# Performance work log

Measured on AMD Instinct MI355X. Metric: run time of the kernel, lower is better.

## Reference

```python
import jax, jax.numpy as jnp
import numpy as np

B, T, DIN, H = 8, 4096, 1024, 2048
INIT_SCALE = 0.1


def setup_inputs() -> dict:
    key = jax.random.key(0)
    ks = jax.random.split(key, 5)
    x = jax.random.normal(ks[0], (B, T, DIN), dtype=jnp.float32)
    Wi = jax.random.normal(ks[1], (H, DIN), dtype=jnp.float32) * INIT_SCALE
    Wg = jax.random.normal(ks[2], (H, DIN), dtype=jnp.float32) * INIT_SCALE
    Wo = jax.random.normal(ks[3], (DIN, H), dtype=jnp.float32) * INIT_SCALE
    log_a = jax.random.normal(ks[4], (H,), dtype=jnp.float32) * INIT_SCALE - 1.0
    bi = jnp.zeros((H,), dtype=jnp.float32)
    bg = jnp.zeros((H,), dtype=jnp.float32)
    bo = jnp.zeros((DIN,), dtype=jnp.float32)
    return {"x": x, "Wi": Wi, "bi": bi, "Wg": Wg, "bg": bg,
            "Wo": Wo, "bo": bo, "log_a": log_a}


def _lru_forward(x, Wi, bi, Wg, bg, Wo, bo, log_a):
    # u, gate: (B, T, H)
    u = jnp.einsum('btd,hd->bth', x, Wi) + bi
    gate = jax.nn.sigmoid(jnp.einsum('btd,hd->bth', x, Wg) + bg)
    a = jax.nn.sigmoid(log_a)  # (H,) diagonal recurrence coefficient

    # diagonal linear recurrence h_t = a*h_{t-1} + u_t, scanned over time
    def step(h, u_t):
        h = a * h + u_t
        return h, h

    u_tbh = jnp.swapaxes(u, 0, 1)  # (T, B, H)
    h0 = jnp.zeros((x.shape[0], log_a.shape[0]), dtype=x.dtype)
    _, h_seq = jax.lax.scan(step, h0, u_tbh)  # (T, B, H)
    h_seq = jnp.swapaxes(h_seq, 0, 1)  # (B, T, H)

    y = jnp.einsum('bth,dh->btd', h_seq * gate, Wo) + bo
    return y


def reference(x, Wi, bi, Wg, bg, Wo, bo, log_a):
    return _lru_forward(x, Wi, bi, Wg, bg, Wo, bo, log_a)
```

## Files before the change

### kernel.cpp

```cpp
#include <hip/hip_runtime.h>
#include <hip/hip_bf16.h>
#include <stdint.h>

using bf16 = __hip_bfloat16;

typedef short bf16x8 __attribute__((ext_vector_type(8)));
typedef float f32x4 __attribute__((ext_vector_type(4)));

__device__ __forceinline__ float bf2f(bf16 x) { return __bfloat162float(x); }
__device__ __forceinline__ bf16 f2bf(float x) { return __float2bfloat16(x); }

__device__ __forceinline__ void async_load16(const bf16* gptr, bf16* lptr) {
    __builtin_amdgcn_global_load_lds(
        (const __attribute__((address_space(1))) void*)gptr,
        (__attribute__((address_space(3))) void*)lptr,
        16, 0, 0);
}

__device__ __forceinline__ void wg_barrier() {
    asm volatile("" ::: "memory");
    __builtin_amdgcn_s_barrier();
    asm volatile("" ::: "memory");
}

#define VMCNT(n) asm volatile("s_waitcnt vmcnt(" #n ")" ::: "memory")

template <int MODE>
__global__ __launch_bounds__(512, 2) void gemm256(
    const bf16* __restrict__ A, const bf16* __restrict__ Bt,
    const float* __restrict__ bias, void* __restrict__ Cout,
    int M, int N, int K)
{
    __shared__ bf16 lds[2 * 2 * 32 * 512];

    const int tid  = threadIdx.x;
    const int wid  = tid >> 6;
    const int lane = tid & 63;
    const int wm = wid >> 2;
    const int wn = wid & 3;

    const int nwg = gridDim.x;
    const int q8 = nwg >> 3, r8 = nwg & 7;
    const int xcd = blockIdx.x & 7, loc = blockIdx.x >> 3;
    const int wgid = (xcd < r8 ? xcd * (q8 + 1) : r8 * (q8 + 1) + (xcd - r8) * q8) + loc;
    const int ntn = N >> 8;
    const int bx = wgid % ntn;
    const int by = wgid / ntn;
    const int m0 = by * 256;
    const int n0 = bx * 256;

    const bf16* Ablk = A  + (size_t)m0 * K;
    const bf16* Bblk = Bt + (size_t)n0 * K;

    const int frow = lane & 15;
    const int fq   = lane >> 4;
    const int roff = frow * 32 + ((fq ^ ((frow >> 1) & 3)) * 8);

    const int swl  = lane ^ ((lane >> 3) & 3);
    const int srow = swl >> 2;
    const int scol = (swl & 3) * 8;

    const int rgA = (wid & 3) + ((wid & 4) << 1);
    const int rgB = (wid & 1) + ((wid & 2) << 1) + ((wid & 4) << 1);

    auto stageA = [&](int buf, int k0, int q) {
        const int rg = rgA + q * 4;
        const bf16* g = Ablk + (size_t)(rg * 16 + srow) * K + (k0 + scol);
        bf16* l = &lds[buf * 32768 + rg * 1024];
        async_load16(g, l);
        async_load16(g + 32, l + 512);
    };
    auto stageB = [&](int buf, int k0, int q) {
        const int rg = rgB + q * 2;
        const bf16* g = Bblk + (size_t)(rg * 16 + srow) * K + (k0 + scol);
        bf16* l = &lds[buf * 32768 + 16384 + rg * 1024];
        async_load16(g, l);
        async_load16(g + 32, l + 512);
    };

    f32x4 acc[8][4];
#pragma unroll
    for (int i = 0; i < 8; ++i)
#pragma unroll
        for (int j = 0; j < 4; ++j)
            acc[i][j] = f32x4{0.f, 0.f, 0.f, 0.f};

    bf16x8 af[4][2];
    bf16x8 bfr[2][2][2];

    auto LDA = [&](int buf, int ih) {
#pragma unroll
        for (int i = 0; i < 4; ++i)
#pragma unroll
            for (int kk = 0; kk < 2; ++kk)
                af[i][kk] = *(const bf16x8*)&lds[buf * 32768 +
                    ((wm * 8 + ih * 4 + i) * 2 + kk) * 512 + roff];
    };
    auto LDB = [&](int buf, int jh) {
#pragma unroll
        for (int j = 0; j < 2; ++j)
#pragma unroll
            for (int kk = 0; kk < 2; ++kk)
                bfr[jh][j][kk] = *(const bf16x8*)&lds[buf * 32768 + 16384 +
                    ((wn * 4 + jh * 2 + j) * 2 + kk) * 512 + roff];
    };
    auto MFMAQ = [&](int ih, int jh) {
        __builtin_amdgcn_s_setprio(1);
#pragma unroll
        for (int kk = 0; kk < 2; ++kk)
#pragma unroll
            for (int i = 0; i < 4; ++i)
#pragma unroll
                for (int j = 0; j < 2; ++j)
                    acc[ih * 4 + i][jh * 2 + j] =
                        __builtin_amdgcn_mfma_f32_16x16x32_bf16(
                            af[i][kk], bfr[jh][j][kk],
                            acc[ih * 4 + i][jh * 2 + j], 0, 0, 0);
        __builtin_amdgcn_s_setprio(0);
    };

    stageA(0, 0, 0);
    stageB(0, 0, 1);
    stageA(0, 0, 1);
    stageB(0, 0, 0);
    stageA(1, 64, 0);
    stageB(1, 64, 1);
    VMCNT(4);
    wg_barrier();

    const int NT = K >> 6;
    for (int t = 0; t < NT; t += 2) {
        const int k1 = (t + 1) << 6;
        const int k2 = (t + 2 < NT ? t + 2 : NT - 1) << 6;
        const int k3 = (t + 3 < NT ? t + 3 : NT - 1) << 6;

        LDA(0, 0); LDB(0, 0);
        stageA(1, k1, 1);
        wg_barrier();
        MFMAQ(0, 0);
        LDB(0, 1);
        stageB(1, k1, 0);
        wg_barrier();
        MFMAQ(0, 1);
        LDA(0, 1);
        stageA(0, k2, 0);
        wg_barrier();
        MFMAQ(1, 1);
        stageB(0, k2, 1);
        VMCNT(4);
        wg_barrier();
        MFMAQ(1, 0);
        LDA(1, 0); LDB(1, 0);
        stageA(0, k2, 1);
        wg_barrier();
        MFMAQ(0, 0);
        LDB(1, 1);
        stageB(0, k2, 0);
        wg_barrier();
        MFMAQ(0, 1);
        LDA(1, 1);
        stageA(1, k3, 0);
        wg_barrier();
        MFMAQ(1, 1);
        stageB(1, k3, 1);
        VMCNT(4);
        wg_barrier();
        MFMAQ(1, 0);
    }
    asm volatile("s_waitcnt vmcnt(0)" ::: "memory");

    const int crow = fq * 4;
    const int ccol = frow;
    float bv[4];
#pragma unroll
    for (int j = 0; j < 4; ++j) bv[j] = bias[n0 + wn * 64 + 16 * j + ccol];
#pragma unroll
    for (int i = 0; i < 8; ++i) {
#pragma unroll
        for (int r = 0; r < 4; ++r) {
            const int row = m0 + wm * 128 + 16 * i + crow + r;
#pragma unroll
            for (int j = 0; j < 4; ++j) {
                const int col = n0 + wn * 64 + 16 * j + ccol;
                float v = acc[i][j][r] + bv[j];
                if constexpr (MODE == 1) v = 1.f / (1.f + __expf(-v));
                if constexpr (MODE == 2)
                    ((float*)Cout)[(size_t)row * N + col] = v;
                else
                    ((bf16*)Cout)[(size_t)row * N + col] = f2bf(v);
            }
        }
    }
}

#define SCAN_T 4096
#define SCAN_H 2048
#define SCAN_B 8
#define SCAN_L 512
#define SCAN_W 64

__global__ __launch_bounds__(256) void lru_scan(
    const bf16* __restrict__ u, bf16* gs, const float* __restrict__ asig)
{
    const int tid   = blockIdx.x * 256 + threadIdx.x;
    const int h     = tid & (SCAN_H - 1);
    const int rem   = tid >> 11;
    const int b     = rem & (SCAN_B - 1);
    const int chunk = rem >> 3;

    const float a = asig[h];
    const size_t base = (size_t)b * SCAN_T * SCAN_H + h;
    const bf16* up = u + base;
    bf16* gp = gs + base;

    const int t1 = chunk * SCAN_L;
    const int warm0 = (chunk == 0) ? 0 : SCAN_W;

    float hs = 0.f;
    for (int t = t1 - warm0; t < t1; t += 8) {
        float uv[8];
#pragma unroll
        for (int i = 0; i < 8; ++i) uv[i] = bf2f(up[(size_t)(t + i) * SCAN_H]);
#pragma unroll
        for (int i = 0; i < 8; ++i) hs = fmaf(a, hs, uv[i]);
    }
    for (int t = t1; t < t1 + SCAN_L; t += 8) {
        float uv[8], gv[8];
#pragma unroll
        for (int i = 0; i < 8; ++i) {
            uv[i] = bf2f(up[(size_t)(t + i) * SCAN_H]);
            gv[i] = bf2f(gp[(size_t)(t + i) * SCAN_H]);
        }
#pragma unroll
        for (int i = 0; i < 8; ++i) {
            hs = fmaf(a, hs, uv[i]);
            gp[(size_t)(t + i) * SCAN_H] = f2bf(hs * gv[i]);
        }
    }
}

__global__ void cvt_f32_bf16_x4(const float* __restrict__ in,
                                bf16* __restrict__ out, int n4)
{
    const int i = blockIdx.x * blockDim.x + threadIdx.x;
    if (i >= n4) return;
    const float4 v = ((const float4*)in)[i];
    bf16 h[4] __attribute__((aligned(8)));
    h[0] = f2bf(v.x); h[1] = f2bf(v.y); h[2] = f2bf(v.z); h[3] = f2bf(v.w);
    ((uint64_t*)out)[i] = *(const uint64_t*)h;
}

__global__ void sigmoid_vec(const float* __restrict__ in,
                            float* __restrict__ out, int n)
{
    const int i = blockIdx.x * blockDim.x + threadIdx.x;
    if (i < n) out[i] = 1.f / (1.f + __expf(-in[i]));
}

extern "C" void kernel_launch(void* const* d_in, const int* in_sizes, int n_in,
                              void* d_out, int out_size, void* d_ws, size_t ws_size,
                              hipStream_t stream)
{
    const float* x     = (const float*)d_in[0];
    const float* Wi    = (const float*)d_in[1];
    const float* bi    = (const float*)d_in[2];
    const float* Wg    = (const float*)d_in[3];
    const float* bg    = (const float*)d_in[4];
    const float* Wo    = (const float*)d_in[5];
    const float* bo    = (const float*)d_in[6];
    const float* log_a = (const float*)d_in[7];
    float* y = (float*)d_out;

    constexpr int Bc = 8, T = 4096, DIN = 1024, H = 2048;
    constexpr int M = Bc * T;

    char* ws = (char*)d_ws;
    size_t off = 0;
    auto alloc = [&](size_t bytes) -> void* {
        void* p = ws + off;
        off += (bytes + 255) & ~(size_t)255;
        return p;
    };
    bf16*  xb   = (bf16*)alloc((size_t)M * DIN * 2);
    bf16*  wib  = (bf16*)alloc((size_t)H * DIN * 2);
    bf16*  wgb  = (bf16*)alloc((size_t)H * DIN * 2);
    bf16*  wob  = (bf16*)alloc((size_t)DIN * H * 2);
    float* asig = (float*)alloc((size_t)H * 4);
    bf16*  u    = (bf16*)alloc((size_t)M * H * 2);
    bf16*  g    = (bf16*)alloc((size_t)M * H * 2);
    (void)ws_size; (void)in_sizes; (void)n_in; (void)out_size;

    {
        const int n4 = M * DIN / 4;
        cvt_f32_bf16_x4<<<(n4 + 255) / 256, 256, 0, stream>>>(x, xb, n4);
        const int w4 = H * DIN / 4;
        cvt_f32_bf16_x4<<<(w4 + 255) / 256, 256, 0, stream>>>(Wi, wib, w4);
        cvt_f32_bf16_x4<<<(w4 + 255) / 256, 256, 0, stream>>>(Wg, wgb, w4);
        cvt_f32_bf16_x4<<<(w4 + 255) / 256, 256, 0, stream>>>(Wo, wob, w4);
        sigmoid_vec<<<(H + 255) / 256, 256, 0, stream>>>(log_a, asig, H);
    }

    gemm256<0><<<(M / 256) * (H / 256), 512, 0, stream>>>(xb, wib, bi, u, M, H, DIN);
    gemm256<1><<<(M / 256) * (H / 256), 512, 0, stream>>>(xb, wgb, bg, g, M, H, DIN);

    lru_scan<<<(Bc * H * (T / SCAN_L)) / 256, 256, 0, stream>>>(u, g, asig);

    gemm256<2><<<(M / 256) * (DIN / 256), 512, 0, stream>>>(g, wob, bo, y, M, DIN, H);
}
```

Baseline: 726.4 us.

## Shrink GEMM tile to 256x128 with 4 waves and single-buffer LDS pipeline

Changes the GEMM workgroup from 512 threads with a 256x256 tile and double-buffered LDS (128KB) to 256 threads with a 256x128 tile and a single 64KB LDS buffer. The A tile's second half alternates between two slots so the next k-tile can be staged while the current one is consumed. The intent is to cut LDS use so more workgroups fit per CU and to double the grid size for better load balance. In exchange, each output element gets less reuse of the loaded data and the schedule has more barriers per k-step and less prefetch depth.

```diff
diff --git a/kernel.cpp b/kernel.cpp
--- a/kernel.cpp
+++ b/kernel.cpp
@@ -26,28 +26,28 @@
 #define VMCNT(n) asm volatile("s_waitcnt vmcnt(" #n ")" ::: "memory")
 
 template <int MODE>
-__global__ __launch_bounds__(512, 2) void gemm256(
+__global__ __launch_bounds__(256, 2) void gemm256(
     const bf16* __restrict__ A, const bf16* __restrict__ Bt,
     const float* __restrict__ bias, void* __restrict__ Cout,
     int M, int N, int K)
 {
-    __shared__ bf16 lds[2 * 2 * 32 * 512];
+    __shared__ bf16 lds[32768];
 
     const int tid  = threadIdx.x;
     const int wid  = tid >> 6;
     const int lane = tid & 63;
-    const int wm = wid >> 2;
-    const int wn = wid & 3;
+    const int wm = wid >> 1;
+    const int wn = wid & 1;
 
     const int nwg = gridDim.x;
     const int q8 = nwg >> 3, r8 = nwg & 7;
     const int xcd = blockIdx.x & 7, loc = blockIdx.x >> 3;
     const int wgid = (xcd < r8 ? xcd * (q8 + 1) : r8 * (q8 + 1) + (xcd - r8) * q8) + loc;
-    const int ntn = N >> 8;
+    const int ntn = N >> 7;
     const int bx = wgid % ntn;
     const int by = wgid / ntn;
     const int m0 = by * 256;
-    const int n0 = bx * 256;
+    const int n0 = bx * 128;
 
     const bf16* Ablk = A  + (size_t)m0 * K;
     const bf16* Bblk = Bt + (size_t)n0 * K;
@@ -60,23 +60,24 @@
     const int srow = swl >> 2;
     const int scol = (swl & 3) * 8;
 
-    const int rgA = (wid & 3) + ((wid & 4) << 1);
-    const int rgB = (wid & 1) + ((wid & 2) << 1) + ((wid & 4) << 1);
-
-    auto stageA = [&](int buf, int k0, int q) {
-        const int rg = rgA + q * 4;
-        const bf16* g = Ablk + (size_t)(rg * 16 + srow) * K + (k0 + scol);
-        bf16* l = &lds[buf * 32768 + rg * 1024];
+    auto stageA = [&](int k0, int q, int slot) {
+#pragma unroll
+        for (int rr = 0; rr < 2; ++rr) {
+            const int r = wid * 2 + rr;
+            const int p = (r & 3) + q * 4 + ((r >> 2) << 3);
+            const bf16* g = Ablk + (size_t)(p * 16 + srow) * K + (k0 + scol);
+            bf16* l = (q == 1 && slot) ? &lds[24576 + r * 1024] : &lds[p * 1024];
+            async_load16(g, l);
+            async_load16(g + 32, l + 512);
+        }
+    };
+    auto stageB = [&](int k0, int q) {
+        const int p = (wid & 1) + ((wid >> 1) << 2) + q * 2;
+        const bf16* g = Bblk + (size_t)(p * 16 + srow) * K + (k0 + scol);
+        bf16* l = &lds[16384 + p * 1024];
         async_load16(g, l);
         async_load16(g + 32, l + 512);
     };
-    auto stageB = [&](int buf, int k0, int q) {
-        const int rg = rgB + q * 2;
-        const bf16* g = Bblk + (size_t)(rg * 16 + srow) * K + (k0 + scol);
-        bf16* l = &lds[buf * 32768 + 16384 + rg * 1024];
-        async_load16(g, l);
-        async_load16(g + 32, l + 512);
-    };
 
     f32x4 acc[8][4];
 #pragma unroll
@@ -88,21 +89,30 @@
     bf16x8 af[4][2];
     bf16x8 bfr[2][2][2];
 
-    auto LDA = [&](int buf, int ih) {
+    auto LDA0 = [&]() {
 #pragma unroll
         for (int i = 0; i < 4; ++i)
 #pragma unroll
             for (int kk = 0; kk < 2; ++kk)
-                af[i][kk] = *(const bf16x8*)&lds[buf * 32768 +
-                    ((wm * 8 + ih * 4 + i) * 2 + kk) * 512 + roff];
-    };
-    auto LDB = [&](int buf, int jh) {
+                af[i][kk] = *(const bf16x8*)&lds[(wm * 8 + i) * 1024 + kk * 512 + roff];
+    };
+    auto LDA1 = [&](int slot) {
+#pragma unroll
+        for (int i = 0; i < 4; ++i) {
+            const int base = slot ? (24576 + (wm * 4 + i) * 1024)
+                                  : ((wm * 8 + 4 + i) * 1024);
+#pragma unroll
+            for (int kk = 0; kk < 2; ++kk)
+                af[i][kk] = *(const bf16x8*)&lds[base + kk * 512 + roff];
+        }
+    };
+    auto LDB = [&](int jh) {
 #pragma unroll
         for (int j = 0; j < 2; ++j)
 #pragma unroll
             for (int kk = 0; kk < 2; ++kk)
-                bfr[jh][j][kk] = *(const bf16x8*)&lds[buf * 32768 + 16384 +
-                    ((wn * 4 + jh * 2 + j) * 2 + kk) * 512 + roff];
+                bfr[jh][j][kk] = *(const bf16x8*)&lds[16384 +
+                    (wn * 4 + jh * 2 + j) * 1024 + kk * 512 + roff];
     };
     auto MFMAQ = [&](int ih, int jh) {
         __builtin_amdgcn_s_setprio(1);
@@ -119,55 +129,39 @@
         __builtin_amdgcn_s_setprio(0);
     };
 
+    const int NT = K >> 6;
+
+    stageA(0, 1, 0);
     stageA(0, 0, 0);
-    stageB(0, 0, 1);
-    stageA(0, 0, 1);
-    stageB(0, 0, 0);
-    stageA(1, 64, 0);
-    stageB(1, 64, 1);
-    VMCNT(4);
+    stageB(0, 0);
+    stageB(0, 1);
+    VMCNT(2);
     wg_barrier();
-
-    const int NT = K >> 6;
-    for (int t = 0; t < NT; t += 2) {
-        const int k1 = (t + 1) << 6;
-        const int k2 = (t + 2 < NT ? t + 2 : NT - 1) << 6;
-        const int k3 = (t + 3 < NT ? t + 3 : NT - 1) << 6;
-
-        LDA(0, 0); LDB(0, 0);
-        stageA(1, k1, 1);
+    LDA0(); LDB(0);
+    VMCNT(0);
+    wg_barrier();
+
+    for (int t = 0; t < NT; ++t) {
+        const int kn = (t + 1 < NT ? t + 1 : NT - 1) << 6;
+        const int sl = (t + 1) & 1;
+        MFMAQ(0, 0);
+        LDB(1);
         wg_barrier();
-        MFMAQ(0, 0);
-        LDB(0, 1);
-        stageB(1, k1, 0);
+        stageA(kn, 1, sl);
+        stageA(kn, 0, 0);
+        stageB(kn, 0);
+        MFMAQ(0, 1);
+        LDA1(t & 1);
         wg_barrier();
-        MFMAQ(0, 1);
-        LDA(0, 1);
-        stageA(0, k2, 0);
-        wg_barrier();
+        stageB(kn, 1);
         MFMAQ(1, 1);
-        stageB(0, k2, 1);
-        VMCNT(4);
+        VMCNT(2);
         wg_barrier();
         MFMAQ(1, 0);
-        LDA(1, 0); LDB(1, 0);
-        stageA(0, k2, 1);
+        LDA0(); LDB(0);
+        VMCNT(0);
         wg_barrier();
-        MFMAQ(0, 0);
-        LDB(1, 1);
-        stageB(0, k2, 0);
-        wg_barrier();
-        MFMAQ(0, 1);
-        LDA(1, 1);
-        stageA(1, k3, 0);
-        wg_barrier();
-        MFMAQ(1, 1);
-        stageB(1, k3, 1);
-        VMCNT(4);
-        wg_barrier();
-        MFMAQ(1, 0);
-    }
-    asm volatile("s_waitcnt vmcnt(0)" ::: "memory");
+    }
 
     const int crow = fq * 4;
     const int ccol = frow;
@@ -300,10 +294,10 @@
         sigmoid_vec<<<(H + 255) / 256, 256, 0, stream>>>(log_a, asig, H);
     }
 
-    gemm256<0><<<(M / 256) * (H / 256), 512, 0, stream>>>(xb, wib, bi, u, M, H, DIN);
-    gemm256<1><<<(M / 256) * (H / 256), 512, 0, stream>>>(xb, wgb, bg, g, M, H, DIN);
+    gemm256<0><<<(M / 256) * (H / 128), 256, 0, stream>>>(xb, wib, bi, u, M, H, DIN);
+    gemm256<1><<<(M / 256) * (H / 128), 256, 0, stream>>>(xb, wgb, bg, g, M, H, DIN);
 
     lru_scan<<<(Bc * H * (T / SCAN_L)) / 256, 256, 0, stream>>>(u, g, asig);
 
-    gemm256<2><<<(M / 256) * (DIN / 256), 512, 0, stream>>>(g, wob, bo, y, M, DIN, H);
-}
+    gemm256<2><<<(M / 256) * (DIN / 128), 256, 0, stream>>>(g, wob, bo, y, M, DIN, H);
+}
```

Result: slower. 753.1 us (+3.7%).

## Replace fine-grained ping-pong GEMM pipeline with simple per-tile double buffering

Applied to the files above, without the earlier changes.

Replaces the unrolled two-tile main loop with a plain double-buffered loop. The old loop interleaved LDS fragment reads, async global-to-LDS staging and MFMA quadrants across eight barrier phases with a partial vmcnt wait. The new loop stages the whole next K-tile at once, runs all four MFMA quadrants, then waits for all loads and synchronises once per tile. It cuts barrier count and scheduling complexity, but loses the overlap of global loads with compute, since each iteration drains outstanding loads before continuing.

```diff
diff --git a/kernel.cpp b/kernel.cpp
--- a/kernel.cpp
+++ b/kernel.cpp
@@ -31,7 +31,7 @@
     const float* __restrict__ bias, void* __restrict__ Cout,
     int M, int N, int K)
 {
-    __shared__ bf16 lds[2 * 2 * 32 * 512];
+    __shared__ bf16 lds[2 * 32768];
 
     const int tid  = threadIdx.x;
     const int wid  = tid >> 6;
@@ -119,55 +119,31 @@
         __builtin_amdgcn_s_setprio(0);
     };
 
+    const int NT = K >> 6;
+
     stageA(0, 0, 0);
-    stageB(0, 0, 1);
     stageA(0, 0, 1);
     stageB(0, 0, 0);
-    stageA(1, 64, 0);
-    stageB(1, 64, 1);
-    VMCNT(4);
+    stageB(0, 0, 1);
+    VMCNT(0);
     wg_barrier();
 
-    const int NT = K >> 6;
-    for (int t = 0; t < NT; t += 2) {
-        const int k1 = (t + 1) << 6;
-        const int k2 = (t + 2 < NT ? t + 2 : NT - 1) << 6;
-        const int k3 = (t + 3 < NT ? t + 3 : NT - 1) << 6;
-
-        LDA(0, 0); LDB(0, 0);
-        stageA(1, k1, 1);
+    for (int t = 0; t < NT; ++t) {
+        const int p  = t & 1;
+        const int kn = (t + 1 < NT ? t + 1 : NT - 1) << 6;
+        LDA(p, 0); LDB(p, 0); LDB(p, 1);
+        stageA(p ^ 1, kn, 0);
+        stageA(p ^ 1, kn, 1);
+        stageB(p ^ 1, kn, 0);
+        stageB(p ^ 1, kn, 1);
+        MFMAQ(0, 0);
+        MFMAQ(0, 1);
+        LDA(p, 1);
+        MFMAQ(1, 1);
+        MFMAQ(1, 0);
+        VMCNT(0);
         wg_barrier();
-        MFMAQ(0, 0);
-        LDB(0, 1);
-        stageB(1, k1, 0);
-        wg_barrier();
-        MFMAQ(0, 1);
-        LDA(0, 1);
-        stageA(0, k2, 0);
-        wg_barrier();
-        MFMAQ(1, 1);
-        stageB(0, k2, 1);
-        VMCNT(4);
-        wg_barrier();
-        MFMAQ(1, 0);
-        LDA(1, 0); LDB(1, 0);
-        stageA(0, k2, 1);
-        wg_barrier();
-        MFMAQ(0, 0);
-        LDB(1, 1);
-        stageB(0, k2, 0);
-        wg_barrier();
-        MFMAQ(0, 1);
-        LDA(1, 1);
-        stageA(1, k3, 0);
-        wg_barrier();
-        MFMAQ(1, 1);
-        stageB(1, k3, 1);
-        VMCNT(4);
-        wg_barrier();
-        MFMAQ(1, 0);
-    }
-    asm volatile("s_waitcnt vmcnt(0)" ::: "memory");
+    }
 
     const int crow = fq * 4;
     const int ccol = frow;
```

New measurement: 749.9 us. +3.2%, slower.
